# Kernel optimization log

Measured on AMD Instinct MI355X. Metric: run time of the kernel, lower is better.

The kernel has to match this reference:

```python
import jax, jax.numpy as jnp
import numpy as np

B, K, D = 16384, 8, 64
NUM_USER, NUM_ENT, NUM_REL = 100000, 1000000, 32


def setup_inputs() -> dict:
    key = jax.random.key(0)
    ks = jax.random.split(key, 12)
    return {
        'u': jax.random.randint(ks[0], (B,), 0, NUM_USER, dtype=jnp.int32),
        'v': jax.random.randint(ks[1], (B,), 0, NUM_ENT, dtype=jnp.int32),
        'user_and_item_adj': jax.random.randint(ks[2], (B, K), 0, NUM_ENT, dtype=jnp.int32),
        'adj_ent': jax.random.randint(ks[3], (NUM_ENT, K), 0, NUM_ENT, dtype=jnp.int32),
        'adj_rel': jax.random.randint(ks[4], (NUM_ENT, K), 0, NUM_REL, dtype=jnp.int32),
        'usr_emb': jax.random.normal(ks[5], (NUM_USER, D), dtype=jnp.float32) * 0.02,
        'ent_emb': jax.random.normal(ks[6], (NUM_ENT, D), dtype=jnp.float32) * 0.02,
        'rel_emb': jax.random.normal(ks[7], (NUM_REL, D), dtype=jnp.float32) * 0.02,
        'conv_w': jax.random.normal(ks[8], (1, K, 3, 3), dtype=jnp.float32) * 0.1,  # OIHW
        'conv_b': jnp.zeros((1,), dtype=jnp.float32),
        'agg_w': jax.random.normal(ks[9], (D, D), dtype=jnp.float32) * 0.05,
        'agg_b': jnp.zeros((D,), dtype=jnp.float32),
    }


def reference(u, v, user_and_item_adj, adj_ent, adj_rel,
              usr_emb, ent_emb, rel_emb, conv_w, conv_b, agg_w, agg_b):
    # --- user-side: user emb * user-item-history entity embs, then conv2d ---
    uai = ent_emb[user_and_item_adj]                      # [B, K, D]
    ue = usr_emb[u][:, None, :] * uai                     # [B, K, D]
    x = ue[..., None]                                     # [B, K, D, 1]  (NCHW)
    y = jax.lax.conv_general_dilated(
        x, conv_w, window_strides=(1, 1), padding=((1, 1), (1, 1)),
        dimension_numbers=('NCHW', 'OIHW', 'NCHW'))      # [B, 1, D, 1]
    user_embeddings = y[:, 0, :, 0] + conv_b[0]           # [B, D]

    # --- item-side: one-hop neighbor gather + KGCN sum aggregator ---
    ent_idx = adj_ent[v]                                  # [B, K]
    rel_idx = adj_rel[v]                                  # [B, K]
    self_vec = ent_emb[v]                                 # [B, D]
    neigh = ent_emb[ent_idx]                              # [B, K, D]
    rels = rel_emb[rel_idx]                               # [B, K, D]

    # user-relation attention scores, softmax over K neighbors
    scores = jnp.einsum('bd,bkd->bk', user_embeddings, rels)   # [B, K]
    attn = jax.nn.softmax(scores, axis=-1)                     # [B, K]
    neigh_agg = jnp.einsum('bk,bkd->bd', attn, neigh)          # [B, D]

    # 'sum' aggregator: (self + neighbors) -> Linear -> sigmoid
    item_embeddings = jax.nn.sigmoid((self_vec + neigh_agg) @ agg_w + agg_b)  # [B, D]

    out = jax.nn.sigmoid(jnp.sum(user_embeddings * item_embeddings, axis=1))  # [B]
    return out
```

## Files before the change

### kernel.cpp

```cpp
#include <hip/hip_runtime.h>
#include <math.h>


__device__ __forceinline__ float4 ld4(const float* p) {
    return *reinterpret_cast<const float4*>(p);
}
__device__ __forceinline__ float dot4(float4 a, float4 b) {
    return fmaf(a.x, b.x, fmaf(a.y, b.y, fmaf(a.z, b.z, a.w * b.w)));
}
__device__ __forceinline__ float4 fma4(float s, float4 a, float4 acc) {
    acc.x = fmaf(s, a.x, acc.x);
    acc.y = fmaf(s, a.y, acc.y);
    acc.z = fmaf(s, a.z, acc.z);
    acc.w = fmaf(s, a.w, acc.w);
    return acc;
}
__device__ __forceinline__ float4 xgroup_sum4(float4 v) {
    v.x += __shfl_xor(v.x, 16, 64); v.x += __shfl_xor(v.x, 32, 64);
    v.y += __shfl_xor(v.y, 16, 64); v.y += __shfl_xor(v.y, 32, 64);
    v.z += __shfl_xor(v.z, 16, 64); v.z += __shfl_xor(v.z, 32, 64);
    v.w += __shfl_xor(v.w, 16, 64); v.w += __shfl_xor(v.w, 32, 64);
    return v;
}
__device__ __forceinline__ float4 shfl4(float4 v, int src) {
    float4 r;
    r.x = __shfl(v.x, src, 64);
    r.y = __shfl(v.y, src, 64);
    r.z = __shfl(v.z, src, 64);
    r.w = __shfl(v.w, src, 64);
    return r;
}

__global__ __launch_bounds__(256) void pifsa_gnn_kernel(
    const int*   __restrict__ u,
    const int*   __restrict__ v,
    const int*   __restrict__ uai,
    const int*   __restrict__ adj_ent,
    const int*   __restrict__ adj_rel,
    const float* __restrict__ usr_emb,
    const float* __restrict__ ent_emb,
    const float* __restrict__ rel_emb,
    const float* __restrict__ conv_w,
    const float* __restrict__ conv_b,
    const float* __restrict__ agg_w,
    const float* __restrict__ agg_b,
    float*       __restrict__ out,
    int B)
{
    const int gtid = blockIdx.x * 256 + threadIdx.x;
    const int b    = gtid >> 6;
    if (b >= B) return;

    const int l  = threadIdx.x & 63;
    const int g  = l >> 4;
    const int q  = l & 15;
    const int d0 = q << 2;

    const int ub = u[b];
    const int vb = v[b];
    const int c0 = g, c1 = g + 4;
    const int e0 = uai[b * 8 + c0];
    const int e1 = uai[b * 8 + c1];
    const int r0 = adj_rel[vb * 8 + c0];
    const int r1 = adj_rel[vb * 8 + c1];
    const int n0 = adj_ent[vb * 8 + c0];
    const int n1 = adj_ent[vb * 8 + c1];

    const float4 usr = ld4(usr_emb + ub * 64 + d0);
    float4 a0 = ld4(ent_emb + (size_t)e0 * 64 + d0);
    float4 a1 = ld4(ent_emb + (size_t)e1 * 64 + d0);
    float4 ue0, ue1;
    ue0.x = usr.x * a0.x; ue0.y = usr.y * a0.y; ue0.z = usr.z * a0.z; ue0.w = usr.w * a0.w;
    ue1.x = usr.x * a1.x; ue1.y = usr.y * a1.y; ue1.z = usr.z * a1.z; ue1.w = usr.w * a1.w;

    const float w0a = conv_w[c0 * 9 + 1], w1a = conv_w[c0 * 9 + 4], w2a = conv_w[c0 * 9 + 7];
    const float w0b = conv_w[c1 * 9 + 1], w1b = conv_w[c1 * 9 + 4], w2b = conv_w[c1 * 9 + 7];

    float4 cacc = make_float4(0.f, 0.f, 0.f, 0.f);
    {
        float pw = __shfl(ue0.w, (l - 1) & 63, 64); if (q == 0)  pw = 0.f;
        float nx = __shfl(ue0.x, (l + 1) & 63, 64); if (q == 15) nx = 0.f;
        float4 prev = make_float4(pw, ue0.x, ue0.y, ue0.z);
        float4 next = make_float4(ue0.y, ue0.z, ue0.w, nx);
        cacc = fma4(w1a, ue0, cacc);
        cacc = fma4(w0a, prev, cacc);
        cacc = fma4(w2a, next, cacc);
    }
    {
        float pw = __shfl(ue1.w, (l - 1) & 63, 64); if (q == 0)  pw = 0.f;
        float nx = __shfl(ue1.x, (l + 1) & 63, 64); if (q == 15) nx = 0.f;
        float4 prev = make_float4(pw, ue1.x, ue1.y, ue1.z);
        float4 next = make_float4(ue1.y, ue1.z, ue1.w, nx);
        cacc = fma4(w1b, ue1, cacc);
        cacc = fma4(w0b, prev, cacc);
        cacc = fma4(w2b, next, cacc);
    }
    cacc = xgroup_sum4(cacc);
    const float cb = conv_b[0];
    float4 user_e = make_float4(cacc.x + cb, cacc.y + cb, cacc.z + cb, cacc.w + cb);

    float p0 = dot4(user_e, ld4(rel_emb + r0 * 64 + d0));
    float p1 = dot4(user_e, ld4(rel_emb + r1 * 64 + d0));
#pragma unroll
    for (int off = 1; off <= 8; off <<= 1) {
        p0 += __shfl_xor(p0, off, 64);
        p1 += __shfl_xor(p1, off, 64);
    }
    float s[8];
#pragma unroll
    for (int kk = 0; kk < 4; ++kk) {
        s[kk]     = __shfl(p0, kk * 16, 64);
        s[kk + 4] = __shfl(p1, kk * 16, 64);
    }

    float m = s[0];
#pragma unroll
    for (int k = 1; k < 8; ++k) m = fmaxf(m, s[k]);
    float den = 0.f;
    float ek[8];
#pragma unroll
    for (int k = 0; k < 8; ++k) { ek[k] = __expf(s[k] - m); den += ek[k]; }
    const float inv_den = 1.f / den;
    const float at0 = ek[c0] * inv_den;
    const float at1 = ek[c1] * inv_den;

    float4 nb0 = ld4(ent_emb + (size_t)n0 * 64 + d0);
    float4 nb1 = ld4(ent_emb + (size_t)n1 * 64 + d0);
    float4 hp = make_float4(0.f, 0.f, 0.f, 0.f);
    hp = fma4(at0, nb0, hp);
    hp = fma4(at1, nb1, hp);
    hp = xgroup_sum4(hp);
    const float4 self4 = ld4(ent_emb + (size_t)vb * 64 + d0);
    float4 h4 = make_float4(self4.x + hp.x, self4.y + hp.y, self4.z + hp.z, self4.w + hp.w);

    float4 acc = make_float4(0.f, 0.f, 0.f, 0.f);
#pragma unroll
    for (int i = 0; i < 4; ++i) {
        const float4 hb = shfl4(h4, 20 * g + i);
        const float* wrow = agg_w + (16 * g + 4 * i) * 64 + d0;
        acc = fma4(hb.x, ld4(wrow),       acc);
        acc = fma4(hb.y, ld4(wrow + 64),  acc);
        acc = fma4(hb.z, ld4(wrow + 128), acc);
        acc = fma4(hb.w, ld4(wrow + 192), acc);
    }
    acc = xgroup_sum4(acc);
    const float4 bias = ld4(agg_b + d0);
    float4 item;
    item.x = 1.f / (1.f + __expf(-(acc.x + bias.x)));
    item.y = 1.f / (1.f + __expf(-(acc.y + bias.y)));
    item.z = 1.f / (1.f + __expf(-(acc.z + bias.z)));
    item.w = 1.f / (1.f + __expf(-(acc.w + bias.w)));

    float p = dot4(user_e, item);
#pragma unroll
    for (int off = 1; off <= 8; off <<= 1)
        p += __shfl_xor(p, off, 64);

    if (l == 0)
        out[b] = 1.f / (1.f + __expf(-p));
}

extern "C" void kernel_launch(void* const* d_in, const int* in_sizes, int n_in,
                              void* d_out, int out_size, void* d_ws, size_t ws_size,
                              hipStream_t stream) {
    const int*   u        = (const int*)  d_in[0];
    const int*   v        = (const int*)  d_in[1];
    const int*   uai      = (const int*)  d_in[2];
    const int*   adj_ent  = (const int*)  d_in[3];
    const int*   adj_rel  = (const int*)  d_in[4];
    const float* usr_emb  = (const float*)d_in[5];
    const float* ent_emb  = (const float*)d_in[6];
    const float* rel_emb  = (const float*)d_in[7];
    const float* conv_w   = (const float*)d_in[8];
    const float* conv_b   = (const float*)d_in[9];
    const float* agg_w    = (const float*)d_in[10];
    const float* agg_b    = (const float*)d_in[11];
    float*       out      = (float*)d_out;

    const int B = in_sizes[0];
    const int grid = (B + 3) / 4;
    pifsa_gnn_kernel<<<grid, 256, 0, stream>>>(
        u, v, uai, adj_ent, adj_rel, usr_emb, ent_emb, rel_emb,
        conv_w, conv_b, agg_w, agg_b, out, B);
}
```

Measured before the change: 357.7 us.

## Process two batch rows per wavefront and hoist all gathers upfront

Each 64-lane wavefront now handles two batch elements instead of one. All index loads and embedding gathers for both rows (user, self, history, neighbor and relation vectors) are issued before any compute, so more memory requests are in flight. The agg_w rows loaded for the linear layer are shared between the two rows. The cost is higher register pressure and half as many wavefronts, which may reduce occupancy-based latency hiding.

After: 359.7 us. Within noise of the previous version (+0.6%).

```diff
diff --git a/kernel.cpp b/kernel.cpp
--- a/kernel.cpp
+++ b/kernel.cpp
@@ -14,6 +14,9 @@
     acc.z = fmaf(s, a.z, acc.z);
     acc.w = fmaf(s, a.w, acc.w);
     return acc;
+}
+__device__ __forceinline__ float4 mul4(float4 a, float4 b) {
+    return make_float4(a.x * b.x, a.y * b.y, a.z * b.z, a.w * b.w);
 }
 __device__ __forceinline__ float4 xgroup_sum4(float4 v) {
     v.x += __shfl_xor(v.x, 16, 64); v.x += __shfl_xor(v.x, 32, 64);
@@ -47,117 +50,144 @@
     float*       __restrict__ out,
     int B)
 {
-    const int gtid = blockIdx.x * 256 + threadIdx.x;
-    const int b    = gtid >> 6;
-    if (b >= B) return;
+    const int widx = (blockIdx.x * 256 + threadIdx.x) >> 6;
+    const int b0   = widx * 2;
+    if (b0 >= B) return;
+    const bool two = (b0 + 1 < B);
 
     const int l  = threadIdx.x & 63;
     const int g  = l >> 4;
     const int q  = l & 15;
     const int d0 = q << 2;
-
-    const int ub = u[b];
-    const int vb = v[b];
     const int c0 = g, c1 = g + 4;
-    const int e0 = uai[b * 8 + c0];
-    const int e1 = uai[b * 8 + c1];
-    const int r0 = adj_rel[vb * 8 + c0];
-    const int r1 = adj_rel[vb * 8 + c1];
-    const int n0 = adj_ent[vb * 8 + c0];
-    const int n1 = adj_ent[vb * 8 + c1];
-
-    const float4 usr = ld4(usr_emb + ub * 64 + d0);
-    float4 a0 = ld4(ent_emb + (size_t)e0 * 64 + d0);
-    float4 a1 = ld4(ent_emb + (size_t)e1 * 64 + d0);
-    float4 ue0, ue1;
-    ue0.x = usr.x * a0.x; ue0.y = usr.y * a0.y; ue0.z = usr.z * a0.z; ue0.w = usr.w * a0.w;
-    ue1.x = usr.x * a1.x; ue1.y = usr.y * a1.y; ue1.z = usr.z * a1.z; ue1.w = usr.w * a1.w;
+
+    int bb[2];
+    bb[0] = b0;
+    bb[1] = two ? b0 + 1 : b0;
+
+    int ub[2], vb[2];
+#pragma unroll
+    for (int t = 0; t < 2; ++t) { ub[t] = u[bb[t]]; vb[t] = v[bb[t]]; }
+
+    int e0[2], e1[2], r0[2], r1[2], n0[2], n1[2];
+#pragma unroll
+    for (int t = 0; t < 2; ++t) {
+        e0[t] = uai[bb[t] * 8 + c0];
+        e1[t] = uai[bb[t] * 8 + c1];
+        r0[t] = adj_rel[vb[t] * 8 + c0];
+        r1[t] = adj_rel[vb[t] * 8 + c1];
+        n0[t] = adj_ent[vb[t] * 8 + c0];
+        n1[t] = adj_ent[vb[t] * 8 + c1];
+    }
+
+    float4 usr[2], self4[2], a0[2], a1[2], nb0[2], nb1[2], re0[2], re1[2];
+#pragma unroll
+    for (int t = 0; t < 2; ++t) {
+        usr[t]   = ld4(usr_emb + (size_t)ub[t] * 64 + d0);
+        self4[t] = ld4(ent_emb + (size_t)vb[t] * 64 + d0);
+        a0[t]    = ld4(ent_emb + (size_t)e0[t] * 64 + d0);
+        a1[t]    = ld4(ent_emb + (size_t)e1[t] * 64 + d0);
+        nb0[t]   = ld4(ent_emb + (size_t)n0[t] * 64 + d0);
+        nb1[t]   = ld4(ent_emb + (size_t)n1[t] * 64 + d0);
+        re0[t]   = ld4(rel_emb + (size_t)r0[t] * 64 + d0);
+        re1[t]   = ld4(rel_emb + (size_t)r1[t] * 64 + d0);
+    }
 
     const float w0a = conv_w[c0 * 9 + 1], w1a = conv_w[c0 * 9 + 4], w2a = conv_w[c0 * 9 + 7];
     const float w0b = conv_w[c1 * 9 + 1], w1b = conv_w[c1 * 9 + 4], w2b = conv_w[c1 * 9 + 7];
-
-    float4 cacc = make_float4(0.f, 0.f, 0.f, 0.f);
-    {
-        float pw = __shfl(ue0.w, (l - 1) & 63, 64); if (q == 0)  pw = 0.f;
-        float nx = __shfl(ue0.x, (l + 1) & 63, 64); if (q == 15) nx = 0.f;
-        float4 prev = make_float4(pw, ue0.x, ue0.y, ue0.z);
-        float4 next = make_float4(ue0.y, ue0.z, ue0.w, nx);
-        cacc = fma4(w1a, ue0, cacc);
-        cacc = fma4(w0a, prev, cacc);
-        cacc = fma4(w2a, next, cacc);
-    }
-    {
-        float pw = __shfl(ue1.w, (l - 1) & 63, 64); if (q == 0)  pw = 0.f;
-        float nx = __shfl(ue1.x, (l + 1) & 63, 64); if (q == 15) nx = 0.f;
-        float4 prev = make_float4(pw, ue1.x, ue1.y, ue1.z);
-        float4 next = make_float4(ue1.y, ue1.z, ue1.w, nx);
-        cacc = fma4(w1b, ue1, cacc);
-        cacc = fma4(w0b, prev, cacc);
-        cacc = fma4(w2b, next, cacc);
-    }
-    cacc = xgroup_sum4(cacc);
-    const float cb = conv_b[0];
-    float4 user_e = make_float4(cacc.x + cb, cacc.y + cb, cacc.z + cb, cacc.w + cb);
-
-    float p0 = dot4(user_e, ld4(rel_emb + r0 * 64 + d0));
-    float p1 = dot4(user_e, ld4(rel_emb + r1 * 64 + d0));
-#pragma unroll
-    for (int off = 1; off <= 8; off <<= 1) {
-        p0 += __shfl_xor(p0, off, 64);
-        p1 += __shfl_xor(p1, off, 64);
-    }
-    float s[8];
-#pragma unroll
-    for (int kk = 0; kk < 4; ++kk) {
-        s[kk]     = __shfl(p0, kk * 16, 64);
-        s[kk + 4] = __shfl(p1, kk * 16, 64);
-    }
-
-    float m = s[0];
-#pragma unroll
-    for (int k = 1; k < 8; ++k) m = fmaxf(m, s[k]);
-    float den = 0.f;
-    float ek[8];
-#pragma unroll
-    for (int k = 0; k < 8; ++k) { ek[k] = __expf(s[k] - m); den += ek[k]; }
-    const float inv_den = 1.f / den;
-    const float at0 = ek[c0] * inv_den;
-    const float at1 = ek[c1] * inv_den;
-
-    float4 nb0 = ld4(ent_emb + (size_t)n0 * 64 + d0);
-    float4 nb1 = ld4(ent_emb + (size_t)n1 * 64 + d0);
-    float4 hp = make_float4(0.f, 0.f, 0.f, 0.f);
-    hp = fma4(at0, nb0, hp);
-    hp = fma4(at1, nb1, hp);
-    hp = xgroup_sum4(hp);
-    const float4 self4 = ld4(ent_emb + (size_t)vb * 64 + d0);
-    float4 h4 = make_float4(self4.x + hp.x, self4.y + hp.y, self4.z + hp.z, self4.w + hp.w);
-
-    float4 acc = make_float4(0.f, 0.f, 0.f, 0.f);
+    const float cb  = conv_b[0];
+    const float4 bias = ld4(agg_b + d0);
+
+    float4 user_e[2], h4[2];
+#pragma unroll
+    for (int t = 0; t < 2; ++t) {
+        float4 ue0 = mul4(usr[t], a0[t]);
+        float4 ue1 = mul4(usr[t], a1[t]);
+
+        float4 cacc = make_float4(0.f, 0.f, 0.f, 0.f);
+        {
+            float pw = __shfl(ue0.w, (l - 1) & 63, 64); if (q == 0)  pw = 0.f;
+            float nx = __shfl(ue0.x, (l + 1) & 63, 64); if (q == 15) nx = 0.f;
+            cacc = fma4(w1a, ue0, cacc);
+            cacc = fma4(w0a, make_float4(pw, ue0.x, ue0.y, ue0.z), cacc);
+            cacc = fma4(w2a, make_float4(ue0.y, ue0.z, ue0.w, nx), cacc);
+        }
+        {
+            float pw = __shfl(ue1.w, (l - 1) & 63, 64); if (q == 0)  pw = 0.f;
+            float nx = __shfl(ue1.x, (l + 1) & 63, 64); if (q == 15) nx = 0.f;
+            cacc = fma4(w1b, ue1, cacc);
+            cacc = fma4(w0b, make_float4(pw, ue1.x, ue1.y, ue1.z), cacc);
+            cacc = fma4(w2b, make_float4(ue1.y, ue1.z, ue1.w, nx), cacc);
+        }
+        cacc = xgroup_sum4(cacc);
+        user_e[t] = make_float4(cacc.x + cb, cacc.y + cb, cacc.z + cb, cacc.w + cb);
+
+        float p0 = dot4(user_e[t], re0[t]);
+        float p1 = dot4(user_e[t], re1[t]);
+#pragma unroll
+        for (int off = 1; off <= 8; off <<= 1) {
+            p0 += __shfl_xor(p0, off, 64);
+            p1 += __shfl_xor(p1, off, 64);
+        }
+        float s[8];
+#pragma unroll
+        for (int kk = 0; kk < 4; ++kk) {
+            s[kk]     = __shfl(p0, kk * 16, 64);
+            s[kk + 4] = __shfl(p1, kk * 16, 64);
+        }
+        float m = s[0];
+#pragma unroll
+        for (int k = 1; k < 8; ++k) m = fmaxf(m, s[k]);
+        float den = 0.f, ek[8];
+#pragma unroll
+        for (int k = 0; k < 8; ++k) { ek[k] = __expf(s[k] - m); den += ek[k]; }
+        const float inv_den = 1.f / den;
+
+        float4 hp = make_float4(0.f, 0.f, 0.f, 0.f);
+        hp = fma4(ek[c0] * inv_den, nb0[t], hp);
+        hp = fma4(ek[c1] * inv_den, nb1[t], hp);
+        hp = xgroup_sum4(hp);
+        h4[t] = make_float4(self4[t].x + hp.x, self4[t].y + hp.y,
+                            self4[t].z + hp.z, self4[t].w + hp.w);
+    }
+
+    float4 acc[2];
+    acc[0] = make_float4(0.f, 0.f, 0.f, 0.f);
+    acc[1] = make_float4(0.f, 0.f, 0.f, 0.f);
 #pragma unroll
     for (int i = 0; i < 4; ++i) {
-        const float4 hb = shfl4(h4, 20 * g + i);
         const float* wrow = agg_w + (16 * g + 4 * i) * 64 + d0;
-        acc = fma4(hb.x, ld4(wrow),       acc);
-        acc = fma4(hb.y, ld4(wrow + 64),  acc);
-        acc = fma4(hb.z, ld4(wrow + 128), acc);
-        acc = fma4(hb.w, ld4(wrow + 192), acc);
-    }
-    acc = xgroup_sum4(acc);
-    const float4 bias = ld4(agg_b + d0);
-    float4 item;
-    item.x = 1.f / (1.f + __expf(-(acc.x + bias.x)));
-    item.y = 1.f / (1.f + __expf(-(acc.y + bias.y)));
-    item.z = 1.f / (1.f + __expf(-(acc.z + bias.z)));
-    item.w = 1.f / (1.f + __expf(-(acc.w + bias.w)));
-
-    float p = dot4(user_e, item);
-#pragma unroll
-    for (int off = 1; off <= 8; off <<= 1)
-        p += __shfl_xor(p, off, 64);
-
-    if (l == 0)
-        out[b] = 1.f / (1.f + __expf(-p));
+        const float4 w0 = ld4(wrow);
+        const float4 w1 = ld4(wrow + 64);
+        const float4 w2 = ld4(wrow + 128);
+        const float4 w3 = ld4(wrow + 192);
+#pragma unroll
+        for (int t = 0; t < 2; ++t) {
+            const float4 hb = shfl4(h4[t], 20 * g + i);
+            acc[t] = fma4(hb.x, w0, acc[t]);
+            acc[t] = fma4(hb.y, w1, acc[t]);
+            acc[t] = fma4(hb.z, w2, acc[t]);
+            acc[t] = fma4(hb.w, w3, acc[t]);
+        }
+    }
+
+#pragma unroll
+    for (int t = 0; t < 2; ++t) {
+        float4 ac = xgroup_sum4(acc[t]);
+        float4 item;
+        item.x = 1.f / (1.f + __expf(-(ac.x + bias.x)));
+        item.y = 1.f / (1.f + __expf(-(ac.y + bias.y)));
+        item.z = 1.f / (1.f + __expf(-(ac.z + bias.z)));
+        item.w = 1.f / (1.f + __expf(-(ac.w + bias.w)));
+
+        float p = dot4(user_e[t], item);
+#pragma unroll
+        for (int off = 1; off <= 8; off <<= 1)
+            p += __shfl_xor(p, off, 64);
+
+        if (l == 0 && (t == 0 || two))
+            out[bb[t]] = 1.f / (1.f + __expf(-p));
+    }
 }
 
 extern "C" void kernel_launch(void* const* d_in, const int* in_sizes, int n_in,
@@ -178,7 +208,8 @@
     float*       out      = (float*)d_out;
 
     const int B = in_sizes[0];
-    const int grid = (B + 3) / 4;
+    const int nwaves = (B + 1) / 2;
+    const int grid   = (nwaves + 3) / 4;
     pifsa_gnn_kernel<<<grid, 256, 0, stream>>>(
         u, v, uai, adj_ent, adj_rel, usr_emb, ent_emb, rel_emb,
         conv_w, conv_b, agg_w, agg_b, out, B);
```
